# Performance work log

Hardware: AMD Instinct MI355X
Metric: run time of the kernel (lower is better)

Reference implementation:

```python
import jax, jax.numpy as jnp
import numpy as np

N = 50000
E = 800000
DIM = 64
MAX_DEG = 64
NUM_LAB = 16
BN_EPS = 1e-5
SLOPE = 0.01


def lrelu(x):
    return jnp.where(x > 0, x, SLOPE * x)


def batchnorm(x, w, b):
    m = x.mean(axis=0)
    v = x.var(axis=0)  # biased, matches torch BN normalization
    return (x - m) * jax.lax.rsqrt(v + BN_EPS) * w + b


def gin_conv(x, src, dst, wa, ba, wb, bb):
    # GINConv (eps=0): mlp(x + sum_{j->i} x_j); mlp = lin -> lrelu -> lin
    agg = jax.ops.segment_sum(x[src], dst, num_segments=x.shape[0])
    h = x + agg
    h = lrelu(h @ wa.T + ba)
    return h @ wb.T + bb


def setup_inputs() -> dict:
    key = jax.random.key(0)
    ks = iter(jax.random.split(key, 64))
    f = lambda *s: (jax.random.normal(next(ks), s, dtype=jnp.float32) * 0.1)
    dims = [2 * DIM, DIM, DIM, DIM]  # [128,64,64,64]
    inp = {
        'emb_deg': f(MAX_DEG, DIM),
        'emb_lab': f(NUM_LAB, DIM),
    }
    for i, (n1, n2) in enumerate(zip(dims[:-1], dims[1:])):
        inp[f'w{i}a'] = f(n1, n1)
        inp[f'b{i}a'] = f(n1)
        inp[f'w{i}b'] = f(n2, n1)
        inp[f'b{i}b'] = f(n2)
        inp[f'bn{i}_w'] = f(n2) + 1.0
        inp[f'bn{i}_b'] = f(n2)
    S = sum(dims)  # 320
    inp['fc1_w'] = f(DIM, S)
    inp['fc1_b'] = f(DIM)
    inp['fcbn_w'] = f(DIM) + 1.0
    inp['fcbn_b'] = f(DIM)
    inp['fc2_w'] = f(1, DIM)
    inp['fc2_b'] = f(1)
    inp['node_deg'] = jax.random.randint(next(ks), (N,), 0, MAX_DEG)
    inp['node_lab'] = jax.random.randint(next(ks), (N,), 0, NUM_LAB)
    inp['edge_index'] = jax.random.randint(next(ks), (2, E), 0, N)
    return inp


def reference(emb_deg, emb_lab,
              w0a, b0a, w0b, b0b, bn0_w, bn0_b,
              w1a, b1a, w1b, b1b, bn1_w, bn1_b,
              w2a, b2a, w2b, b2b, bn2_w, bn2_b,
              fc1_w, fc1_b, fcbn_w, fcbn_b, fc2_w, fc2_b,
              node_deg, node_lab, edge_index):
    src, dst = edge_index[0], edge_index[1]
    x0 = jnp.concatenate([emb_deg[node_deg], emb_lab[node_lab]], axis=1)  # [N, 2*DIM]
    z = [x0]
    layers = [(w0a, b0a, w0b, b0b, bn0_w, bn0_b),
              (w1a, b1a, w1b, b1b, bn1_w, bn1_b),
              (w2a, b2a, w2b, b2b, bn2_w, bn2_b)]
    for wa, ba, wb, bb, gw, gb in layers:
        x = gin_conv(z[-1], src, dst, wa, ba, wb, bb)
        x = lrelu(batchnorm(x, gw, gb))
        z.append(x)
    x = jnp.concatenate(z, axis=1)  # [N, sum(dims)]
    h = x @ fc1_w.T + fc1_b
    h = lrelu(batchnorm(h, fcbn_w, fcbn_b))
    out = jax.nn.sigmoid(h @ fc2_w.T + fc2_b)
    return out.squeeze(-1)  # [N]
```

## Files before the change

### kernel.cpp

```cpp
#include <hip/hip_runtime.h>

#define N_NODES 50000
#define E_EDGES 800000
#define BN_EPS 1e-5f
#define SLOPE 0.01f

#define SCAN_CHUNK 2048
#define SCAN_BLOCKS ((N_NODES + SCAN_CHUNK - 1) / SCAN_CHUNK)
#define STAT_SHARDS 32

typedef unsigned short ushort_t;
typedef unsigned int uint_t;
typedef short short8 __attribute__((ext_vector_type(8)));
typedef float floatx4 __attribute__((ext_vector_type(4)));

__device__ __forceinline__ float b2f(ushort_t v) {
    return __uint_as_float(((uint_t)v) << 16);
}
__device__ __forceinline__ float ulo(uint_t v) {
    return __uint_as_float(v << 16);
}
__device__ __forceinline__ float uhi(uint_t v) {
    return __uint_as_float(v & 0xffff0000u);
}
__device__ __forceinline__ ushort_t f2b(float f) {
    uint_t u = __float_as_uint(f);
    return (ushort_t)((u + 0x7fffu + ((u >> 16) & 1u)) >> 16);
}
__device__ __forceinline__ uint_t pack2(float a, float b) {
    return (uint_t)f2b(a) | ((uint_t)f2b(b) << 16);
}

#define OWA0 0
#define OWB0 16384
#define OWA1 24576
#define OWB1 28672
#define OWA2 32768
#define OWB2 36864
#define OFC1 40960
#define WTOT 61440

__global__ void k_cvt(const float* __restrict__ wa0, const float* __restrict__ wb0,
                      const float* __restrict__ wa1, const float* __restrict__ wb1,
                      const float* __restrict__ wa2, const float* __restrict__ wb2,
                      const float* __restrict__ fc1w, ushort_t* __restrict__ dst) {
    int i = blockIdx.x * blockDim.x + threadIdx.x;
    if (i >= WTOT) return;
    float v;
    if      (i < OWB0) v = wa0[i];
    else if (i < OWA1) v = wb0[i - OWB0];
    else if (i < OWB1) v = wa1[i - OWA1];
    else if (i < OWA2) v = wb1[i - OWB1];
    else if (i < OWB2) v = wa2[i - OWA2];
    else if (i < OFC1) v = wb2[i - OWB2];
    else               v = fc1w[i - OFC1];
    dst[i] = f2b(v);
}

__global__ void k_build_x0(const float* __restrict__ ed, const float* __restrict__ el,
                           const int* __restrict__ nd, const int* __restrict__ nl,
                           uint_t* __restrict__ x0u, int* __restrict__ ncls) {
    int idx = blockIdx.x * blockDim.x + threadIdx.x;
    if (idx >= N_NODES * 64) return;
    int n = idx >> 6, c = idx & 63;
    int d = nd[n], l = nl[n];
    if (c == 0) ncls[n] = d | (l << 16);
    float2 v = (c < 32) ? *(const float2*)(ed + d * 64 + c * 2)
                        : *(const float2*)(el + l * 64 + (c - 32) * 2);
    x0u[(size_t)n * 64 + c] = pack2(v.x, v.y);
}

__global__ void k_deg(const int* __restrict__ dst, int* __restrict__ deg) {
    int e = blockIdx.x * blockDim.x + threadIdx.x;
    if (e >= E_EDGES) return;
    atomicAdd(&deg[dst[e]], 1);
}

__global__ __launch_bounds__(256) void k_scan_a(const int* __restrict__ deg,
                                                int* __restrict__ bsum) {
    __shared__ int wsum[4];
    int t = threadIdx.x, b = blockIdx.x;
    int base = b * SCAN_CHUNK + t * 8;
    int s = 0;
    #pragma unroll
    for (int i = 0; i < 8; ++i) {
        int idx = base + i;
        if (idx < N_NODES) s += deg[idx];
    }
    #pragma unroll
    for (int o = 32; o; o >>= 1) s += __shfl_down(s, o);
    if ((t & 63) == 0) wsum[t >> 6] = s;
    __syncthreads();
    if (t == 0) bsum[b] = wsum[0] + wsum[1] + wsum[2] + wsum[3];
}

__global__ void k_scan_b(const int* __restrict__ bsum, int* __restrict__ bofs) {
    int t = threadIdx.x;
    int v = (t < SCAN_BLOCKS) ? bsum[t] : 0;
    int inc = v;
    #pragma unroll
    for (int o = 1; o < 32; o <<= 1) {
        int u = __shfl_up(inc, o, 32);
        if ((t & 31) >= o) inc += u;
    }
    if (t < SCAN_BLOCKS) bofs[t] = inc - v;
}

__global__ __launch_bounds__(256) void k_scan_c(const int* __restrict__ deg,
        const int* __restrict__ bofs, int* __restrict__ rowptr, int* __restrict__ wptr) {
    __shared__ int part[256];
    int t = threadIdx.x, b = blockIdx.x;
    int base = b * SCAN_CHUNK + t * 8;
    int vals[8];
    int s = 0;
    #pragma unroll
    for (int i = 0; i < 8; ++i) {
        int idx = base + i;
        vals[i] = (idx < N_NODES) ? deg[idx] : 0;
        s += vals[i];
    }
    part[t] = s;
    __syncthreads();
    #pragma unroll
    for (int off = 1; off < 256; off <<= 1) {
        int v = (t >= off) ? part[t - off] : 0;
        __syncthreads();
        part[t] += v;
        __syncthreads();
    }
    int run = bofs[b] + part[t] - s;
    #pragma unroll
    for (int i = 0; i < 8; ++i) {
        int idx = base + i;
        if (idx < N_NODES) {
            rowptr[idx] = run;
            wptr[idx]   = run;
            run += vals[i];
        }
    }
}

__global__ void k_fill(const int* __restrict__ src, const int* __restrict__ dst,
                       const int* __restrict__ ncls,
                       int* __restrict__ wptr, int2* __restrict__ ebuf) {
    int e = blockIdx.x * blockDim.x + threadIdx.x;
    if (e >= E_EDGES) return;
    int s = src[e];
    int pos = atomicAdd(&wptr[dst[e]], 1);
    ebuf[pos] = make_int2(s, ncls[s]);
}

template<int D>
__global__ __launch_bounds__(256, 8) void k_mlp(
        const ushort_t* __restrict__ xb,
        const int* __restrict__ rowptr, const int* __restrict__ cdeg,
        const int2* __restrict__ ebuf, const int* __restrict__ ncls,
        const float* __restrict__ ed, const float* __restrict__ el,
        const ushort_t* __restrict__ waB, const float* __restrict__ ba,
        const ushort_t* __restrict__ wbB, const float* __restrict__ bb,
        float* __restrict__ ybuf, float* __restrict__ stat_l) {
    constexpr int LDWB = D + 8;
    __shared__ ushort_t xs[16 * LDWB];
    __shared__ ushort_t hs[16 * LDWB];
    int t = threadIdx.x;
    int row0 = blockIdx.x * 16;
    int lane = t & 63, wv = t >> 6;
    int half = lane >> 5, hl = lane & 31;
    uint_t* xsu = (uint_t*)xs;

    if constexpr (D == 128) {
        bool lo = hl < 16;
        const float* tab = lo ? ed : el;
        int dcol = (lo ? hl : hl - 16) * 4;
        for (int i = 0; i < 2; ++i) {
            int lr = wv * 4 + i * 2 + half, node = row0 + lr;
            float ax = 0.f, ay = 0.f, az = 0.f, aw = 0.f;
            float bx = 0.f, by = 0.f, bz = 0.f, bw = 0.f;
            if (node < N_NODES) {
                int start = rowptr[node], n = cdeg[node];
                int scls = ncls[node];
                int d = lo ? (scls & 0xffff) : (scls >> 16);
                float4 v = *(const float4*)(tab + d * 64 + dcol);
                ax = v.x; ay = v.y; az = v.z; aw = v.w;
                for (int j0 = 0; j0 < n; j0 += 32) {
                    int m = n - j0; if (m > 32) m = 32;
                    int clsv = (hl < m) ? ebuf[start + j0 + hl].y : 0;
                    int j = 0;
                    for (; j + 2 <= m; j += 2) {
                        int c0 = __shfl(clsv, j, 32), c1 = __shfl(clsv, j + 1, 32);
                        int d0 = lo ? (c0 & 0xffff) : (c0 >> 16);
                        int d1 = lo ? (c1 & 0xffff) : (c1 >> 16);
                        float4 v0 = *(const float4*)(tab + d0 * 64 + dcol);
                        float4 v1 = *(const float4*)(tab + d1 * 64 + dcol);
                        ax += v0.x; ay += v0.y; az += v0.z; aw += v0.w;
                        bx += v1.x; by += v1.y; bz += v1.z; bw += v1.w;
                    }
                    if (j < m) {
                        int c0 = __shfl(clsv, j, 32);
                        int d0 = lo ? (c0 & 0xffff) : (c0 >> 16);
                        float4 v0 = *(const float4*)(tab + d0 * 64 + dcol);
                        ax += v0.x; ay += v0.y; az += v0.z; aw += v0.w;
                    }
                }
            }
            xsu[lr * (LDWB / 2) + hl * 2]     = pack2(ax + bx, ay + by);
            xsu[lr * (LDWB / 2) + hl * 2 + 1] = pack2(az + bz, aw + bw);
        }
    } else {
        const uint_t* xu = (const uint_t*)xb;
        for (int i = 0; i < 2; ++i) {
            int lr = wv * 4 + i * 2 + half, node = row0 + lr;
            float a0 = 0.f, a1 = 0.f, b0 = 0.f, b1 = 0.f;
            float c0f = 0.f, c1f = 0.f, d0f = 0.f, d1f = 0.f;
            if (node < N_NODES) {
                int start = rowptr[node], n = cdeg[node];
                uint_t sv = xu[(size_t)node * 32 + hl];
                a0 = ulo(sv); a1 = uhi(sv);
                for (int j0 = 0; j0 < n; j0 += 32) {
                    int m = n - j0; if (m > 32) m = 32;
                    int ev = (hl < m) ? ebuf[start + j0 + hl].x : 0;
                    int j = 0;
                    for (; j + 4 <= m; j += 4) {
                        int s0 = __shfl(ev, j, 32),     s1 = __shfl(ev, j + 1, 32);
                        int s2 = __shfl(ev, j + 2, 32), s3 = __shfl(ev, j + 3, 32);
                        uint_t v0 = xu[(size_t)s0 * 32 + hl];
                        uint_t v1 = xu[(size_t)s1 * 32 + hl];
                        uint_t v2 = xu[(size_t)s2 * 32 + hl];
                        uint_t v3 = xu[(size_t)s3 * 32 + hl];
                        a0 += ulo(v0); a1 += uhi(v0);
                        b0 += ulo(v1); b1 += uhi(v1);
                        c0f += ulo(v2); c1f += uhi(v2);
                        d0f += ulo(v3); d1f += uhi(v3);
                    }
                    for (; j < m; ++j) {
                        int s0 = __shfl(ev, j, 32);
                        uint_t v0 = xu[(size_t)s0 * 32 + hl];
                        a0 += ulo(v0); a1 += uhi(v0);
                    }
                }
            }
            xsu[lr * (LDWB / 2) + hl] = pack2((a0 + b0) + (c0f + d0f),
                                              (a1 + b1) + (c1f + d1f));
        }
    }
    __syncthreads();

    int m = lane & 15, quad = lane >> 4;
    constexpr int NKS = D / 32;
    constexpr int NG1 = D / 64;

    {
        floatx4 acc[NG1];
        #pragma unroll
        for (int g = 0; g < NG1; ++g) acc[g] = (floatx4){0.f, 0.f, 0.f, 0.f};
        #pragma unroll
        for (int ks = 0; ks < NKS; ++ks) {
            short8 af = *(const short8*)(xs + m * LDWB + ks * 32 + quad * 8);
            #pragma unroll
            for (int g = 0; g < NG1; ++g) {
                int col = (wv * NG1 + g) * 16 + m;
                short8 bf = *(const short8*)(waB + (size_t)col * D + ks * 32 + quad * 8);
                acc[g] = __builtin_amdgcn_mfma_f32_16x16x32_bf16(af, bf, acc[g], 0, 0, 0);
            }
        }
        #pragma unroll
        for (int g = 0; g < NG1; ++g) {
            int col = (wv * NG1 + g) * 16 + m;
            float bias = ba[col];
            #pragma unroll
            for (int r = 0; r < 4; ++r) {
                float v = acc[g][r] + bias;
                v = v > 0.f ? v : SLOPE * v;
                hs[(quad * 4 + r) * LDWB + col] = f2b(v);
            }
        }
    }
    __syncthreads();

    {
        floatx4 acc = (floatx4){0.f, 0.f, 0.f, 0.f};
        int col = wv * 16 + m;
        #pragma unroll
        for (int ks = 0; ks < NKS; ++ks) {
            short8 af = *(const short8*)(hs + m * LDWB + ks * 32 + quad * 8);
            short8 bf = *(const short8*)(wbB + (size_t)col * D + ks * 32 + quad * 8);
            acc = __builtin_amdgcn_mfma_f32_16x16x32_bf16(af, bf, acc, 0, 0, 0);
        }
        float bias = bb[col];
        float ps = 0.f, pq = 0.f;
        #pragma unroll
        for (int r = 0; r < 4; ++r) {
            int node = row0 + quad * 4 + r;
            float v = acc[r] + bias;
            if (node < N_NODES) ybuf[(size_t)node * 64 + col] = v;
            else v = 0.f;
            ps += v; pq += v * v;
        }
        ps += __shfl_xor(ps, 16); pq += __shfl_xor(pq, 16);
        ps += __shfl_xor(ps, 32); pq += __shfl_xor(pq, 32);
        if (quad == 0) {
            float* st = stat_l + (blockIdx.x & (STAT_SHARDS - 1)) * 128;
            atomicAdd(&st[col], ps);
            atomicAdd(&st[64 + col], pq);
        }
    }
}

__global__ void k_bn_apply(const float* __restrict__ y, const float* __restrict__ stat_l,
                           const float* __restrict__ gw, const float* __restrict__ gb,
                           uint_t* __restrict__ xo) {
    __shared__ float sc[64], sh[64];
    int t = threadIdx.x;
    if (t < 64) {
        float s0 = 0.f, q0 = 0.f;
        #pragma unroll
        for (int j = 0; j < STAT_SHARDS; ++j) {
            s0 += stat_l[j * 128 + t];
            q0 += stat_l[j * 128 + 64 + t];
        }
        float mmm = s0 * (1.0f / N_NODES);
        float var = q0 * (1.0f / N_NODES) - mmm * mmm;
        float s = gw[t] * rsqrtf(var + BN_EPS);
        sc[t] = s; sh[t] = gb[t] - mmm * s;
    }
    __syncthreads();
    int idx = blockIdx.x * blockDim.x + t;
    if (idx >= N_NODES * 16) return;
    int c4 = (idx & 15) * 4;
    float4 v4 = *(const float4*)(y + (size_t)idx * 4);
    float o0 = v4.x * sc[c4]     + sh[c4];     o0 = o0 > 0.f ? o0 : SLOPE * o0;
    float o1 = v4.y * sc[c4 + 1] + sh[c4 + 1]; o1 = o1 > 0.f ? o1 : SLOPE * o1;
    float o2 = v4.z * sc[c4 + 2] + sh[c4 + 2]; o2 = o2 > 0.f ? o2 : SLOPE * o2;
    float o3 = v4.w * sc[c4 + 3] + sh[c4 + 3]; o3 = o3 > 0.f ? o3 : SLOPE * o3;
    xo[(size_t)idx * 2]     = pack2(o0, o1);
    xo[(size_t)idx * 2 + 1] = pack2(o2, o3);
}

__global__ __launch_bounds__(256, 8) void k_fc1(
        const uint_t* __restrict__ x0u, const uint_t* __restrict__ x1u,
        const uint_t* __restrict__ x2u, const uint_t* __restrict__ x3u,
        const ushort_t* __restrict__ wB, const float* __restrict__ b,
        float* __restrict__ ybuf, float* __restrict__ stat_l) {
    constexpr int LDWB = 328;
    __shared__ ushort_t xs[16 * LDWB];
    uint_t* xsu = (uint_t*)xs;
    int t = threadIdx.x;
    int row0 = blockIdx.x * 16;

    for (int i = t; i < 16 * 160; i += 256) {
        int row = i / 160, c = i % 160;
        int g = row0 + row;
        uint_t v = 0;
        if (g < N_NODES) {
            if      (c < 64)  v = x0u[(size_t)g * 64 + c];
            else if (c < 96)  v = x1u[(size_t)g * 32 + (c - 64)];
            else if (c < 128) v = x2u[(size_t)g * 32 + (c - 96)];
            else              v = x3u[(size_t)g * 32 + (c - 128)];
        }
        xsu[row * 164 + c] = v;
    }
    __syncthreads();

    int lane = t & 63, wv = t >> 6;
    int m = lane & 15, quad = lane >> 4;
    int col = wv * 16 + m;
    floatx4 acc = (floatx4){0.f, 0.f, 0.f, 0.f};
    #pragma unroll
    for (int ks = 0; ks < 10; ++ks) {
        short8 af = *(const short8*)(xs + m * LDWB + ks * 32 + quad * 8);
        short8 bf = *(const short8*)(wB + (size_t)col * 320 + ks * 32 + quad * 8);
        acc = __builtin_amdgcn_mfma_f32_16x16x32_bf16(af, bf, acc, 0, 0, 0);
    }
    float bias = b[col];
    float ps = 0.f, pq = 0.f;
    #pragma unroll
    for (int r = 0; r < 4; ++r) {
        int node = row0 + quad * 4 + r;
        float v = acc[r] + bias;
        if (node < N_NODES) ybuf[(size_t)node * 64 + col] = v;
        else v = 0.f;
        ps += v; pq += v * v;
    }
    ps += __shfl_xor(ps, 16); pq += __shfl_xor(pq, 16);
    ps += __shfl_xor(ps, 32); pq += __shfl_xor(pq, 32);
    if (quad == 0) {
        float* st = stat_l + (blockIdx.x & (STAT_SHARDS - 1)) * 128;
        atomicAdd(&st[col], ps);
        atomicAdd(&st[64 + col], pq);
    }
}

__global__ void k_final(const float* __restrict__ y, const float* __restrict__ stat_l,
                        const float* __restrict__ gw, const float* __restrict__ gb,
                        const float* __restrict__ w2, const float* __restrict__ b2,
                        float* __restrict__ out) {
    __shared__ float sc[64], sh[64], w[64];
    int t = threadIdx.x;
    if (t < 64) {
        float s0 = 0.f, q0 = 0.f;
        #pragma unroll
        for (int j = 0; j < STAT_SHARDS; ++j) {
            s0 += stat_l[j * 128 + t];
            q0 += stat_l[j * 128 + 64 + t];
        }
        float mmm = s0 * (1.0f / N_NODES);
        float var = q0 * (1.0f / N_NODES) - mmm * mmm;
        float s = gw[t] * rsqrtf(var + BN_EPS);
        sc[t] = s; sh[t] = gb[t] - mmm * s; w[t] = w2[t];
    }
    __syncthreads();
    int i = blockIdx.x * blockDim.x + t;
    if (i >= N_NODES) return;
    float z = b2[0];
    const float* row = y + (size_t)i * 64;
    #pragma unroll
    for (int c = 0; c < 64; c += 4) {
        float4 v4 = *(const float4*)(row + c);
        float v;
        v = v4.x * sc[c]   + sh[c];   v = v > 0.f ? v : SLOPE * v; z += v * w[c];
        v = v4.y * sc[c+1] + sh[c+1]; v = v > 0.f ? v : SLOPE * v; z += v * w[c+1];
        v = v4.z * sc[c+2] + sh[c+2]; v = v > 0.f ? v : SLOPE * v; z += v * w[c+2];
        v = v4.w * sc[c+3] + sh[c+3]; v = v > 0.f ? v : SLOPE * v; z += v * w[c+3];
    }
    out[i] = 1.f / (1.f + __expf(-z));
}

extern "C" void kernel_launch(void* const* d_in, const int* in_sizes, int n_in,
                              void* d_out, int out_size, void* d_ws, size_t ws_size,
                              hipStream_t stream) {
    const float* emb_deg = (const float*)d_in[0];
    const float* emb_lab = (const float*)d_in[1];
    const float* wA[3]  = {(const float*)d_in[2],  (const float*)d_in[8],  (const float*)d_in[14]};
    const float* bA[3]  = {(const float*)d_in[3],  (const float*)d_in[9],  (const float*)d_in[15]};
    const float* wB[3]  = {(const float*)d_in[4],  (const float*)d_in[10], (const float*)d_in[16]};
    const float* bB[3]  = {(const float*)d_in[5],  (const float*)d_in[11], (const float*)d_in[17]};
    const float* bnw[3] = {(const float*)d_in[6],  (const float*)d_in[12], (const float*)d_in[18]};
    const float* bnb[3] = {(const float*)d_in[7],  (const float*)d_in[13], (const float*)d_in[19]};
    const float* fc1_w  = (const float*)d_in[20];
    const float* fc1_b  = (const float*)d_in[21];
    const float* fcbn_w = (const float*)d_in[22];
    const float* fcbn_b = (const float*)d_in[23];
    const float* fc2_w  = (const float*)d_in[24];
    const float* fc2_b  = (const float*)d_in[25];
    const int* node_deg = (const int*)d_in[26];
    const int* node_lab = (const int*)d_in[27];
    const int* src = (const int*)d_in[28];
    const int* dst = src + E_EDGES;
    float* out = (float*)d_out;

    float* ws   = (float*)d_ws;
    float* ybf  = ws;
    float* stat = ybf + (size_t)N_NODES * 64;
    uint_t* x0u = (uint_t*)(stat + 4 * STAT_SHARDS * 128);
    uint_t* x1u = x0u + (size_t)N_NODES * 64;
    uint_t* x2u = x1u + (size_t)N_NODES * 32;
    uint_t* x3u = x2u + (size_t)N_NODES * 32;
    int2* ebuf  = (int2*)(x3u + (size_t)N_NODES * 32);
    ushort_t* wbf = (ushort_t*)(ebuf + E_EDGES);
    int* cdeg   = (int*)(wbf + WTOT);
    int* rowptr = cdeg + N_NODES;
    int* wptr   = rowptr + N_NODES;
    int* ncls   = wptr + N_NODES;
    int* bsum   = ncls + N_NODES;
    int* bofs   = bsum + SCAN_BLOCKS;

    const int RB = (N_NODES + 15) / 16;
    const int VB = (N_NODES * 16 + 255) / 256;
    const int HB = (N_NODES * 64 + 255) / 256;
    const int EB = (E_EDGES + 255) / 256;
    const int NB = (N_NODES + 255) / 256;

    hipMemsetAsync(stat, 0, (size_t)(4 * STAT_SHARDS * 128) * sizeof(float), stream);
    hipMemsetAsync(cdeg, 0, (size_t)N_NODES * sizeof(int), stream);

    k_cvt<<<(WTOT + 255) / 256, 256, 0, stream>>>(wA[0], wB[0], wA[1], wB[1],
                                                  wA[2], wB[2], fc1_w, wbf);
    k_build_x0<<<HB, 256, 0, stream>>>(emb_deg, emb_lab, node_deg, node_lab, x0u, ncls);

    k_deg<<<EB, 256, 0, stream>>>(dst, cdeg);
    k_scan_a<<<SCAN_BLOCKS, 256, 0, stream>>>(cdeg, bsum);
    k_scan_b<<<1, 64, 0, stream>>>(bsum, bofs);
    k_scan_c<<<SCAN_BLOCKS, 256, 0, stream>>>(cdeg, bofs, rowptr, wptr);
    k_fill<<<EB, 256, 0, stream>>>(src, dst, ncls, wptr, ebuf);

    const ushort_t* waOfs[3] = {wbf + OWA0, wbf + OWA1, wbf + OWA2};
    const ushort_t* wbOfs[3] = {wbf + OWB0, wbf + OWB1, wbf + OWB2};
    uint_t* xin[4] = {x0u, x1u, x2u, x3u};
    for (int l = 0; l < 3; ++l) {
        float* st = stat + l * STAT_SHARDS * 128;
        if (l == 0)
            k_mlp<128><<<RB, 256, 0, stream>>>((const ushort_t*)xin[l], rowptr, cdeg,
                ebuf, ncls, emb_deg, emb_lab,
                waOfs[l], bA[l], wbOfs[l], bB[l], ybf, st);
        else
            k_mlp<64><<<RB, 256, 0, stream>>>((const ushort_t*)xin[l], rowptr, cdeg,
                ebuf, ncls, emb_deg, emb_lab,
                waOfs[l], bA[l], wbOfs[l], bB[l], ybf, st);
        k_bn_apply<<<VB, 256, 0, stream>>>(ybf, st, bnw[l], bnb[l], xin[l + 1]);
    }

    float* stf = stat + 3 * STAT_SHARDS * 128;
    k_fc1<<<RB, 256, 0, stream>>>(x0u, x1u, x2u, x3u, wbf + OFC1, fc1_b, ybf, stf);
    k_final<<<NB, 256, 0, stream>>>(ybf, stf, fcbn_w, fcbn_b, fc2_w, fc2_b, out);
}
```

Before: 376.4 us.

## Precompute layer-0 embedding projection and aggregate via per-node class counts

Layer 0's input is a concatenation of two embedding lookups, so its aggregated input equals a count vector over 64 degree and 16 label classes. The change precomputes P = emb × W0a in a prep kernel, builds an 80-wide count matrix per node with atomics, and runs layer 0 as a small count × P MFMA instead of gathering embedding rows per edge. It also shrinks the edge buffer to source ids only and unrolls the layer 1-2 gather by 8. The cost is a 16 MB count buffer plus its memset, two extra float atomics per edge, and counts rounded to bf16, which stay exact only up to 256.

```diff
diff --git a/kernel.cpp b/kernel.cpp
--- a/kernel.cpp
+++ b/kernel.cpp
@@ -14,15 +14,8 @@
 typedef short short8 __attribute__((ext_vector_type(8)));
 typedef float floatx4 __attribute__((ext_vector_type(4)));
 
-__device__ __forceinline__ float b2f(ushort_t v) {
-    return __uint_as_float(((uint_t)v) << 16);
-}
-__device__ __forceinline__ float ulo(uint_t v) {
-    return __uint_as_float(v << 16);
-}
-__device__ __forceinline__ float uhi(uint_t v) {
-    return __uint_as_float(v & 0xffff0000u);
-}
+__device__ __forceinline__ float ulo(uint_t v) { return __uint_as_float(v << 16); }
+__device__ __forceinline__ float uhi(uint_t v) { return __uint_as_float(v & 0xffff0000u); }
 __device__ __forceinline__ ushort_t f2b(float f) {
     uint_t u = __float_as_uint(f);
     return (ushort_t)((u + 0x7fffu + ((u >> 16) & 1u)) >> 16);
@@ -39,41 +32,74 @@
 #define OWB2 36864
 #define OFC1 40960
 #define WTOT 61440
-
-__global__ void k_cvt(const float* __restrict__ wa0, const float* __restrict__ wb0,
-                      const float* __restrict__ wa1, const float* __restrict__ wb1,
-                      const float* __restrict__ wa2, const float* __restrict__ wb2,
-                      const float* __restrict__ fc1w, ushort_t* __restrict__ dst) {
-    int i = blockIdx.x * blockDim.x + threadIdx.x;
-    if (i >= WTOT) return;
-    float v;
-    if      (i < OWB0) v = wa0[i];
-    else if (i < OWA1) v = wb0[i - OWB0];
-    else if (i < OWB1) v = wa1[i - OWA1];
-    else if (i < OWA2) v = wb1[i - OWB1];
-    else if (i < OWB2) v = wa2[i - OWA2];
-    else if (i < OFC1) v = wb2[i - OWB2];
-    else               v = fc1w[i - OFC1];
-    dst[i] = f2b(v);
+#define CVT_BLOCKS ((WTOT + 255) / 256)
+#define P_BLOCKS 48
+
+__global__ void k_prep(const float* __restrict__ wa0, const float* __restrict__ wb0,
+                       const float* __restrict__ wa1, const float* __restrict__ wb1,
+                       const float* __restrict__ wa2, const float* __restrict__ wb2,
+                       const float* __restrict__ fc1w, ushort_t* __restrict__ dst,
+                       const float* __restrict__ ed, const float* __restrict__ el,
+                       ushort_t* __restrict__ P) {
+    int b = blockIdx.x, t = threadIdx.x;
+    if (b < CVT_BLOCKS) {
+        int i = b * 256 + t;
+        if (i >= WTOT) return;
+        float v;
+        if      (i < OWB0) v = wa0[i];
+        else if (i < OWA1) v = wb0[i - OWB0];
+        else if (i < OWB1) v = wa1[i - OWA1];
+        else if (i < OWA2) v = wb1[i - OWB1];
+        else if (i < OWB2) v = wa2[i - OWA2];
+        else if (i < OFC1) v = wb2[i - OWB2];
+        else               v = fc1w[i - OFC1];
+        dst[i] = f2b(v);
+    } else {
+        int pid = (b - CVT_BLOCKS) * 256 + t;
+        int c = pid >> 7, j = pid & 127;
+        float acc = 0.f;
+        if (c < 64) {
+            const float* dr = ed + c * 64;
+            const float* wr = wa0 + (size_t)j * 128;
+            #pragma unroll 8
+            for (int k = 0; k < 64; ++k) acc += dr[k] * wr[k];
+        } else if (c < 80) {
+            const float* dr = el + (c - 64) * 64;
+            const float* wr = wa0 + (size_t)j * 128 + 64;
+            #pragma unroll 8
+            for (int k = 0; k < 64; ++k) acc += dr[k] * wr[k];
+        }
+        P[c * 128 + j] = f2b(acc);
+    }
 }
 
 __global__ void k_build_x0(const float* __restrict__ ed, const float* __restrict__ el,
                            const int* __restrict__ nd, const int* __restrict__ nl,
-                           uint_t* __restrict__ x0u, int* __restrict__ ncls) {
+                           uint_t* __restrict__ x0u, int* __restrict__ ncls,
+                           float* __restrict__ cnt) {
     int idx = blockIdx.x * blockDim.x + threadIdx.x;
     if (idx >= N_NODES * 64) return;
     int n = idx >> 6, c = idx & 63;
     int d = nd[n], l = nl[n];
-    if (c == 0) ncls[n] = d | (l << 16);
+    if (c == 0) {
+        ncls[n] = d | (l << 16);
+        cnt[(size_t)n * 80 + d] = 1.f;
+        cnt[(size_t)n * 80 + 64 + l] = 1.f;
+    }
     float2 v = (c < 32) ? *(const float2*)(ed + d * 64 + c * 2)
                         : *(const float2*)(el + l * 64 + (c - 32) * 2);
     x0u[(size_t)n * 64 + c] = pack2(v.x, v.y);
 }
 
-__global__ void k_deg(const int* __restrict__ dst, int* __restrict__ deg) {
+__global__ void k_degcnt(const int* __restrict__ src, const int* __restrict__ dst,
+                         const int* __restrict__ ncls,
+                         int* __restrict__ deg, float* __restrict__ cnt) {
     int e = blockIdx.x * blockDim.x + threadIdx.x;
     if (e >= E_EDGES) return;
-    atomicAdd(&deg[dst[e]], 1);
+    int d = dst[e], c = ncls[src[e]];
+    atomicAdd(&deg[d], 1);
+    atomicAdd(&cnt[(size_t)d * 80 + (c & 0xffff)], 1.f);
+    atomicAdd(&cnt[(size_t)d * 80 + 64 + (c >> 16)], 1.f);
 }
 
 __global__ __launch_bounds__(256) void k_scan_a(const int* __restrict__ deg,
@@ -141,25 +167,109 @@
 }
 
 __global__ void k_fill(const int* __restrict__ src, const int* __restrict__ dst,
-                       const int* __restrict__ ncls,
-                       int* __restrict__ wptr, int2* __restrict__ ebuf) {
+                       int* __restrict__ wptr, int* __restrict__ eid) {
     int e = blockIdx.x * blockDim.x + threadIdx.x;
     if (e >= E_EDGES) return;
-    int s = src[e];
     int pos = atomicAdd(&wptr[dst[e]], 1);
-    ebuf[pos] = make_int2(s, ncls[s]);
-}
-
-template<int D>
-__global__ __launch_bounds__(256, 8) void k_mlp(
+    eid[pos] = src[e];
+}
+
+__global__ __launch_bounds__(256, 8) void k_mlp0(
+        const float* __restrict__ cnt,
+        const ushort_t* __restrict__ P, const float* __restrict__ ba,
+        const ushort_t* __restrict__ wbB, const float* __restrict__ bb,
+        float* __restrict__ ybuf, float* __restrict__ stat_l) {
+    constexpr int LDC = 104;
+    constexpr int LDH = 136;
+    __shared__ ushort_t xs[16 * LDC];
+    __shared__ ushort_t hs[16 * LDH];
+    uint_t* xsu = (uint_t*)xs;
+    int t = threadIdx.x;
+    int row0 = blockIdx.x * 16;
+
+    for (int i = t; i < 16 * 52; i += 256) {
+        int row = i / 52, c2 = i % 52;
+        int g = row0 + row;
+        uint_t v = 0;
+        if (g < N_NODES && c2 < 40) {
+            float2 cv = *(const float2*)(cnt + (size_t)g * 80 + c2 * 2);
+            v = pack2(cv.x, cv.y);
+        }
+        xsu[row * 52 + c2] = v;
+    }
+    __syncthreads();
+
+    int lane = t & 63, wv = t >> 6;
+    int m = lane & 15, quad = lane >> 4;
+
+    {
+        floatx4 acc[2];
+        acc[0] = (floatx4){0.f, 0.f, 0.f, 0.f};
+        acc[1] = (floatx4){0.f, 0.f, 0.f, 0.f};
+        #pragma unroll
+        for (int ks = 0; ks < 3; ++ks) {
+            short8 af = *(const short8*)(xs + m * LDC + ks * 32 + quad * 8);
+            #pragma unroll
+            for (int g = 0; g < 2; ++g) {
+                int col = (wv * 2 + g) * 16 + m;
+                short8 bf;
+                #pragma unroll
+                for (int j = 0; j < 8; ++j)
+                    bf[j] = *(const short*)(P + (size_t)(ks * 32 + quad * 8 + j) * 128 + col);
+                acc[g] = __builtin_amdgcn_mfma_f32_16x16x32_bf16(af, bf, acc[g], 0, 0, 0);
+            }
+        }
+        #pragma unroll
+        for (int g = 0; g < 2; ++g) {
+            int col = (wv * 2 + g) * 16 + m;
+            float bias = ba[col];
+            #pragma unroll
+            for (int r = 0; r < 4; ++r) {
+                float v = acc[g][r] + bias;
+                v = v > 0.f ? v : SLOPE * v;
+                hs[(quad * 4 + r) * LDH + col] = f2b(v);
+            }
+        }
+    }
+    __syncthreads();
+
+    {
+        floatx4 acc = (floatx4){0.f, 0.f, 0.f, 0.f};
+        int col = wv * 16 + m;
+        #pragma unroll
+        for (int ks = 0; ks < 4; ++ks) {
+            short8 af = *(const short8*)(hs + m * LDH + ks * 32 + quad * 8);
+            short8 bf = *(const short8*)(wbB + (size_t)col * 128 + ks * 32 + quad * 8);
+            acc = __builtin_amdgcn_mfma_f32_16x16x32_bf16(af, bf, acc, 0, 0, 0);
+        }
+        float bias = bb[col];
+        float ps = 0.f, pq = 0.f;
+        #pragma unroll
+        for (int r = 0; r < 4; ++r) {
+            int node = row0 + quad * 4 + r;
+            float v = acc[r] + bias;
+            if (node < N_NODES) ybuf[(size_t)node * 64 + col] = v;
+            else v = 0.f;
+            ps += v; pq += v * v;
+        }
+        ps += __shfl_xor(ps, 16); pq += __shfl_xor(pq, 16);
+        ps += __shfl_xor(ps, 32); pq += __shfl_xor(pq, 32);
+        if (quad == 0) {
+            float* st = stat_l + (blockIdx.x & (STAT_SHARDS - 1)) * 128;
+            atomicAdd(&st[col], ps);
+            atomicAdd(&st[64 + col], pq);
+        }
+    }
+}
+
+__global__ __launch_bounds__(256, 8) void k_mlp64(
         const ushort_t* __restrict__ xb,
         const int* __restrict__ rowptr, const int* __restrict__ cdeg,
-        const int2* __restrict__ ebuf, const int* __restrict__ ncls,
-        const float* __restrict__ ed, const float* __restrict__ el,
+        const int* __restrict__ eid,
         const ushort_t* __restrict__ waB, const float* __restrict__ ba,
         const ushort_t* __restrict__ wbB, const float* __restrict__ bb,
         float* __restrict__ ybuf, float* __restrict__ stat_l) {
-    constexpr int LDWB = D + 8;
+    constexpr int LDWB = 72;
     __shared__ ushort_t xs[16 * LDWB];
     __shared__ ushort_t hs[16 * LDWB];
     int t = threadIdx.x;
@@ -167,123 +277,81 @@
     int lane = t & 63, wv = t >> 6;
     int half = lane >> 5, hl = lane & 31;
     uint_t* xsu = (uint_t*)xs;
-
-    if constexpr (D == 128) {
-        bool lo = hl < 16;
-        const float* tab = lo ? ed : el;
-        int dcol = (lo ? hl : hl - 16) * 4;
-        for (int i = 0; i < 2; ++i) {
-            int lr = wv * 4 + i * 2 + half, node = row0 + lr;
-            float ax = 0.f, ay = 0.f, az = 0.f, aw = 0.f;
-            float bx = 0.f, by = 0.f, bz = 0.f, bw = 0.f;
-            if (node < N_NODES) {
-                int start = rowptr[node], n = cdeg[node];
-                int scls = ncls[node];
-                int d = lo ? (scls & 0xffff) : (scls >> 16);
-                float4 v = *(const float4*)(tab + d * 64 + dcol);
-                ax = v.x; ay = v.y; az = v.z; aw = v.w;
-                for (int j0 = 0; j0 < n; j0 += 32) {
-                    int m = n - j0; if (m > 32) m = 32;
-                    int clsv = (hl < m) ? ebuf[start + j0 + hl].y : 0;
-                    int j = 0;
-                    for (; j + 2 <= m; j += 2) {
-                        int c0 = __shfl(clsv, j, 32), c1 = __shfl(clsv, j + 1, 32);
-                        int d0 = lo ? (c0 & 0xffff) : (c0 >> 16);
-                        int d1 = lo ? (c1 & 0xffff) : (c1 >> 16);
-                        float4 v0 = *(const float4*)(tab + d0 * 64 + dcol);
-                        float4 v1 = *(const float4*)(tab + d1 * 64 + dcol);
-                        ax += v0.x; ay += v0.y; az += v0.z; aw += v0.w;
-                        bx += v1.x; by += v1.y; bz += v1.z; bw += v1.w;
-                    }
-                    if (j < m) {
-                        int c0 = __shfl(clsv, j, 32);
-                        int d0 = lo ? (c0 & 0xffff) : (c0 >> 16);
-                        float4 v0 = *(const float4*)(tab + d0 * 64 + dcol);
-                        ax += v0.x; ay += v0.y; az += v0.z; aw += v0.w;
-                    }
+    const uint_t* xu = (const uint_t*)xb;
+
+    for (int i = 0; i < 2; ++i) {
+        int lr = wv * 4 + i * 2 + half, node = row0 + lr;
+        float a0 = 0.f, a1 = 0.f, b0 = 0.f, b1 = 0.f;
+        float c0 = 0.f, c1 = 0.f, d0 = 0.f, d1 = 0.f;
+        float e0 = 0.f, e1 = 0.f, f0 = 0.f, f1 = 0.f;
+        float g0 = 0.f, g1 = 0.f, h0 = 0.f, h1 = 0.f;
+        if (node < N_NODES) {
+            int start = rowptr[node], n = cdeg[node];
+            uint_t sv = xu[(size_t)node * 32 + hl];
+            a0 = ulo(sv); a1 = uhi(sv);
+            for (int j0 = 0; j0 < n; j0 += 32) {
+                int m = n - j0; if (m > 32) m = 32;
+                int ev = (hl < m) ? eid[start + j0 + hl] : 0;
+                int j = 0;
+                for (; j + 8 <= m; j += 8) {
+                    int s0 = __shfl(ev, j, 32),     s1 = __shfl(ev, j + 1, 32);
+                    int s2 = __shfl(ev, j + 2, 32), s3 = __shfl(ev, j + 3, 32);
+                    int s4 = __shfl(ev, j + 4, 32), s5 = __shfl(ev, j + 5, 32);
+                    int s6 = __shfl(ev, j + 6, 32), s7 = __shfl(ev, j + 7, 32);
+                    uint_t v0 = xu[(size_t)s0 * 32 + hl];
+                    uint_t v1 = xu[(size_t)s1 * 32 + hl];
+                    uint_t v2 = xu[(size_t)s2 * 32 + hl];
+                    uint_t v3 = xu[(size_t)s3 * 32 + hl];
+                    uint_t v4 = xu[(size_t)s4 * 32 + hl];
+                    uint_t v5 = xu[(size_t)s5 * 32 + hl];
+                    uint_t v6 = xu[(size_t)s6 * 32 + hl];
+                    uint_t v7 = xu[(size_t)s7 * 32 + hl];
+                    a0 += ulo(v0); a1 += uhi(v0); b0 += ulo(v1); b1 += uhi(v1);
+                    c0 += ulo(v2); c1 += uhi(v2); d0 += ulo(v3); d1 += uhi(v3);
+                    e0 += ulo(v4); e1 += uhi(v4); f0 += ulo(v5); f1 += uhi(v5);
+                    g0 += ulo(v6); g1 += uhi(v6); h0 += ulo(v7); h1 += uhi(v7);
+                }
+                for (; j < m; ++j) {
+                    int s0 = __shfl(ev, j, 32);
+                    uint_t v0 = xu[(size_t)s0 * 32 + hl];
+                    a0 += ulo(v0); a1 += uhi(v0);
                 }
             }
-            xsu[lr * (LDWB / 2) + hl * 2]     = pack2(ax + bx, ay + by);
-            xsu[lr * (LDWB / 2) + hl * 2 + 1] = pack2(az + bz, aw + bw);
-        }
-    } else {
-        const uint_t* xu = (const uint_t*)xb;
-        for (int i = 0; i < 2; ++i) {
-            int lr = wv * 4 + i * 2 + half, node = row0 + lr;
-            float a0 = 0.f, a1 = 0.f, b0 = 0.f, b1 = 0.f;
-            float c0f = 0.f, c1f = 0.f, d0f = 0.f, d1f = 0.f;
-            if (node < N_NODES) {
-                int start = rowptr[node], n = cdeg[node];
-                uint_t sv = xu[(size_t)node * 32 + hl];
-                a0 = ulo(sv); a1 = uhi(sv);
-                for (int j0 = 0; j0 < n; j0 += 32) {
-                    int m = n - j0; if (m > 32) m = 32;
-                    int ev = (hl < m) ? ebuf[start + j0 + hl].x : 0;
-                    int j = 0;
-                    for (; j + 4 <= m; j += 4) {
-                        int s0 = __shfl(ev, j, 32),     s1 = __shfl(ev, j + 1, 32);
-                        int s2 = __shfl(ev, j + 2, 32), s3 = __shfl(ev, j + 3, 32);
-                        uint_t v0 = xu[(size_t)s0 * 32 + hl];
-                        uint_t v1 = xu[(size_t)s1 * 32 + hl];
-                        uint_t v2 = xu[(size_t)s2 * 32 + hl];
-                        uint_t v3 = xu[(size_t)s3 * 32 + hl];
-                        a0 += ulo(v0); a1 += uhi(v0);
-                        b0 += ulo(v1); b1 += uhi(v1);
-                        c0f += ulo(v2); c1f += uhi(v2);
-                        d0f += ulo(v3); d1f += uhi(v3);
-                    }
-                    for (; j < m; ++j) {
-                        int s0 = __shfl(ev, j, 32);
-                        uint_t v0 = xu[(size_t)s0 * 32 + hl];
-                        a0 += ulo(v0); a1 += uhi(v0);
-                    }
-                }
-            }
-            xsu[lr * (LDWB / 2) + hl] = pack2((a0 + b0) + (c0f + d0f),
-                                              (a1 + b1) + (c1f + d1f));
-        }
+        }
+        float lo = ((a0 + b0) + (c0 + d0)) + ((e0 + f0) + (g0 + h0));
+        float hi = ((a1 + b1) + (c1 + d1)) + ((e1 + f1) + (g1 + h1));
+        xsu[lr * (LDWB / 2) + hl] = pack2(lo, hi);
     }
     __syncthreads();
 
     int m = lane & 15, quad = lane >> 4;
-    constexpr int NKS = D / 32;
-    constexpr int NG1 = D / 64;
-
-    {
-        floatx4 acc[NG1];
-        #pragma unroll
-        for (int g = 0; g < NG1; ++g) acc[g] = (floatx4){0.f, 0.f, 0.f, 0.f};
-        #pragma unroll
-        for (int ks = 0; ks < NKS; ++ks) {
-            short8 af = *(const short8*)(xs + m * LDWB + ks * 32 + quad * 8);
-            #pragma unroll
-            for (int g = 0; g < NG1; ++g) {
-                int col = (wv * NG1 + g) * 16 + m;
-                short8 bf = *(const short8*)(waB + (size_t)col * D + ks * 32 + quad * 8);
-                acc[g] = __builtin_amdgcn_mfma_f32_16x16x32_bf16(af, bf, acc[g], 0, 0, 0);
-            }
-        }
-        #pragma unroll
-        for (int g = 0; g < NG1; ++g) {
-            int col = (wv * NG1 + g) * 16 + m;
-            float bias = ba[col];
-            #pragma unroll
-            for (int r = 0; r < 4; ++r) {
-                float v = acc[g][r] + bias;
-                v = v > 0.f ? v : SLOPE * v;
-                hs[(quad * 4 + r) * LDWB + col] = f2b(v);
-            }
-        }
-    }
-    __syncthreads();
 
     {
         floatx4 acc = (floatx4){0.f, 0.f, 0.f, 0.f};
         int col = wv * 16 + m;
         #pragma unroll
-        for (int ks = 0; ks < NKS; ++ks) {
+        for (int ks = 0; ks < 2; ++ks) {
+            short8 af = *(const short8*)(xs + m * LDWB + ks * 32 + quad * 8);
+            short8 bf = *(const short8*)(waB + (size_t)col * 64 + ks * 32 + quad * 8);
+            acc = __builtin_amdgcn_mfma_f32_16x16x32_bf16(af, bf, acc, 0, 0, 0);
+        }
+        float bias = ba[col];
+        #pragma unroll
+        for (int r = 0; r < 4; ++r) {
+            float v = acc[r] + bias;
+            v = v > 0.f ? v : SLOPE * v;
+            hs[(quad * 4 + r) * LDWB + col] = f2b(v);
+        }
+    }
+    __syncthreads();
+
+    {
+        floatx4 acc = (floatx4){0.f, 0.f, 0.f, 0.f};
+        int col = wv * 16 + m;
+        #pragma unroll
+        for (int ks = 0; ks < 2; ++ks) {
             short8 af = *(const short8*)(hs + m * LDWB + ks * 32 + quad * 8);
-            short8 bf = *(const short8*)(wbB + (size_t)col * D + ks * 32 + quad * 8);
+            short8 bf = *(const short8*)(wbB + (size_t)col * 64 + ks * 32 + quad * 8);
             acc = __builtin_amdgcn_mfma_f32_16x16x32_bf16(af, bf, acc, 0, 0, 0);
         }
         float bias = bb[col];
@@ -451,13 +519,15 @@
     float* ws   = (float*)d_ws;
     float* ybf  = ws;
     float* stat = ybf + (size_t)N_NODES * 64;
-    uint_t* x0u = (uint_t*)(stat + 4 * STAT_SHARDS * 128);
+    float* cnt  = stat + 4 * STAT_SHARDS * 128;
+    uint_t* x0u = (uint_t*)(cnt + (size_t)N_NODES * 80);
     uint_t* x1u = x0u + (size_t)N_NODES * 64;
     uint_t* x2u = x1u + (size_t)N_NODES * 32;
     uint_t* x3u = x2u + (size_t)N_NODES * 32;
-    int2* ebuf  = (int2*)(x3u + (size_t)N_NODES * 32);
-    ushort_t* wbf = (ushort_t*)(ebuf + E_EDGES);
-    int* cdeg   = (int*)(wbf + WTOT);
+    int* eid    = (int*)(x3u + (size_t)N_NODES * 32);
+    ushort_t* wbf = (ushort_t*)(eid + E_EDGES);
+    ushort_t* Pb  = wbf + WTOT;
+    int* cdeg   = (int*)(Pb + 96 * 128);
     int* rowptr = cdeg + N_NODES;
     int* wptr   = rowptr + N_NODES;
     int* ncls   = wptr + N_NODES;
@@ -471,31 +541,30 @@
     const int NB = (N_NODES + 255) / 256;
 
     hipMemsetAsync(stat, 0, (size_t)(4 * STAT_SHARDS * 128) * sizeof(float), stream);
+    hipMemsetAsync(cnt, 0, (size_t)N_NODES * 80 * sizeof(float), stream);
     hipMemsetAsync(cdeg, 0, (size_t)N_NODES * sizeof(int), stream);
 
-    k_cvt<<<(WTOT + 255) / 256, 256, 0, stream>>>(wA[0], wB[0], wA[1], wB[1],
-                                                  wA[2], wB[2], fc1_w, wbf);
-    k_build_x0<<<HB, 256, 0, stream>>>(emb_deg, emb_lab, node_deg, node_lab, x0u, ncls);
-
-    k_deg<<<EB, 256, 0, stream>>>(dst, cdeg);
+    k_prep<<<CVT_BLOCKS + P_BLOCKS, 256, 0, stream>>>(wA[0], wB[0], wA[1], wB[1],
+        wA[2], wB[2], fc1_w, wbf, emb_deg, emb_lab, Pb);
+    k_build_x0<<<HB, 256, 0, stream>>>(emb_deg, emb_lab, node_deg, node_lab,
+                                       x0u, ncls, cnt);
+
+    k_degcnt<<<EB, 256, 0, stream>>>(src, dst, ncls, cdeg, cnt);
     k_scan_a<<<SCAN_BLOCKS, 256, 0, stream>>>(cdeg, bsum);
     k_scan_b<<<1, 64, 0, stream>>>(bsum, bofs);
     k_scan_c<<<SCAN_BLOCKS, 256, 0, stream>>>(cdeg, bofs, rowptr, wptr);
-    k_fill<<<EB, 256, 0, stream>>>(src, dst, ncls, wptr, ebuf);
-
+    k_fill<<<EB, 256, 0, stream>>>(src, dst, wptr, eid);
+
+    k_mlp0<<<RB, 256, 0, stream>>>(cnt, Pb, bA[0], wbf + OWB0, bB[0], ybf, stat);
+    k_bn_apply<<<VB, 256, 0, stream>>>(ybf, stat, bnw[0], bnb[0], x1u);
+
+    uint_t* xin[4] = {x0u, x1u, x2u, x3u};
     const ushort_t* waOfs[3] = {wbf + OWA0, wbf + OWA1, wbf + OWA2};
     const ushort_t* wbOfs[3] = {wbf + OWB0, wbf + OWB1, wbf + OWB2};
-    uint_t* xin[4] = {x0u, x1u, x2u, x3u};
-    for (int l = 0; l < 3; ++l) {
+    for (int l = 1; l < 3; ++l) {
         float* st = stat + l * STAT_SHARDS * 128;
-        if (l == 0)
-            k_mlp<128><<<RB, 256, 0, stream>>>((const ushort_t*)xin[l], rowptr, cdeg,
-                ebuf, ncls, emb_deg, emb_lab,
-                waOfs[l], bA[l], wbOfs[l], bB[l], ybf, st);
-        else
-            k_mlp<64><<<RB, 256, 0, stream>>>((const ushort_t*)xin[l], rowptr, cdeg,
-                ebuf, ncls, emb_deg, emb_lab,
-                waOfs[l], bA[l], wbOfs[l], bB[l], ybf, st);
+        k_mlp64<<<RB, 256, 0, stream>>>((const ushort_t*)xin[l], rowptr, cdeg, eid,
+            waOfs[l], bA[l], wbOfs[l], bB[l], ybf, st);
         k_bn_apply<<<VB, 256, 0, stream>>>(ybf, st, bnw[l], bnb[l], xin[l + 1]);
     }
 
```

After: 435.7 us. +15.8%, slower.
